# Optimization experiments

Hardware: AMD Instinct MI355X
Metric: run time of the kernel (lower is better)

The kernel has to match this reference:

```python
import jax, jax.numpy as jnp
import numpy as np

CUTOFF = 5.0           # module init kwarg
NSYS, NAT = 64, 1000   # 64 systems of 1000 atoms each
BOX = 21.544           # cubic box edge -> ~0.1 atoms/A^3 (water-like density)
MAX_PAIRS = 2_200_000


def setup_inputs() -> dict:
    key = jax.random.key(0)
    coords = jax.random.uniform(key, (NSYS * NAT, 3), dtype=jnp.float32) * BOX
    isys = jnp.repeat(jnp.arange(NSYS, dtype=jnp.int32), NAT)
    natoms = jnp.full((NSYS,), NAT, dtype=jnp.int32)
    return {"coordinates": coords, "isys": isys, "natoms": natoms}


def reference(coordinates, isys, natoms):
    # Fixed-capacity cutoff neighbor list (no PBC branch), faithful to
    # GraphGeneratorFixed: half-list (i<j, same system), squared distances d12,
    # compacted into a MAX_PAIRS buffer padded with padding_value=N, then
    # symmetrized by concatenation.
    nsys = natoms.shape[0]
    n = coordinates.shape[0]
    nat = n // nsys                      # equal-sized systems (static)
    padding_value = n
    cutoff2 = jnp.float32(CUTOFF * CUTOFF)

    x = coordinates.reshape(nsys, nat, 3)                 # [S, nat, 3]
    sq = jnp.sum(x * x, axis=-1)                          # [S, nat]
    gram = jnp.einsum('sid,sjd->sij', x, x)               # [S, nat, nat]
    d12 = sq[:, :, None] + sq[:, None, :] - 2.0 * gram    # squared distances

    triu = jnp.triu(jnp.ones((nat, nat), dtype=bool), k=1)  # i < j half-list
    mask = (d12 < cutoff2) & triu[None, :, :]             # [S, nat, nat]
    mflat = mask.reshape(-1)                              # [S*nat*nat]
    npairs = jnp.sum(mflat)

    # stream-compaction: position of each kept pair in the output buffer
    pos = jnp.cumsum(mflat.astype(jnp.int32)) - 1
    sel = jnp.where(mflat, pos, MAX_PAIRS)                # OOB -> dropped
    flat_idx = jnp.arange(nsys * nat * nat, dtype=jnp.int32)
    idx_buf = jnp.full((MAX_PAIRS,), -1, dtype=jnp.int32).at[sel].set(
        flat_idx, mode='drop')

    valid = idx_buf >= 0
    ib = jnp.maximum(idx_buf, 0)
    s = ib // (nat * nat)
    rem = ib % (nat * nat)
    i = rem // nat
    j = rem % nat
    src = jnp.where(valid, s * nat + i, padding_value)
    dst = jnp.where(valid, s * nat + j, padding_value)
    d12_sel = jnp.where(valid, d12.reshape(-1)[ib], cutoff2)

    # symmetrize (directed graph), as in the original
    edge_src = jnp.concatenate([src, dst])
    edge_dst = jnp.concatenate([dst, src])
    d12_out = jnp.concatenate([d12_sel, d12_sel])
    return edge_src, edge_dst, d12_out, npairs
```

## Files before the change

### kernel.cpp

```cpp
#include <hip/hip_runtime.h>

#define NSYS 64
#define NAT  1000
#define NTOT (NSYS * NAT)
#define MP   2200000
#define CUT2 25.0f
#define PADV 64000.0f
#define SCAN_BLOCKS 250
#define CAP  104
#define EB   512
#define LCN  1152
#define NROWS 512
#define POSB  4096

__device__ __forceinline__ float dist2f(float xi, float yi, float zi,
                                        float xj, float yj, float zj) {
    float dx = xi - xj, dy = yi - yj, dz = zi - zj;
    return fmaf(dz, dz, fmaf(dy, dy, dx * dx));
}

__device__ __forceinline__ int mbcnt(unsigned long long m) {
    unsigned lo = __builtin_amdgcn_mbcnt_lo((unsigned)m, 0u);
    return (int)__builtin_amdgcn_mbcnt_hi((unsigned)(m >> 32), lo);
}

__device__ __forceinline__ int emit_group(uint2* __restrict__ q, int running,
                                          bool k, int j, int r, float d,
                                          unsigned long long m) {
    if (k) {
        int rank = running + mbcnt(m);
        if (rank < CAP)
            q[rank] = make_uint2((unsigned)(j - r), __float_as_uint(d));
    }
    return running + (int)__popcll(m);
}

__global__ __launch_bounds__(1024) void k_eval(const float* __restrict__ coords,
                                               int* __restrict__ counts,
                                               uint2* __restrict__ qbuf) {
    __shared__ float4 lc[LCN];
    int s      = blockIdx.x >> 3;
    int stripe = blockIdx.x & 7;
    const float* cs = coords + s * (NAT * 3);
    for (int a = threadIdx.x; a < LCN; a += 1024)
        lc[a] = (a < NAT)
              ? make_float4(cs[3 * a], cs[3 * a + 1], cs[3 * a + 2], 0.0f)
              : make_float4(1.0e30f, 1.0e30f, 1.0e30f, 0.0f);
    __syncthreads();
    int w    = threadIdx.x >> 6;
    int lane = threadIdx.x & 63;
    int W    = stripe * 16 + w;
    for (int t = 0;; t++) {
        int r = ((t & 1) ? (127 - W) : W) + (t << 7);
        if (r >= NAT) { if (((t & 1) ? W : (127 - W)) + (t << 7) >= NAT) break; else continue; }
        float4 ci = lc[r];
        int grow = s * NAT + r;
        uint2* q = qbuf + (size_t)grow * CAP;
        int running = 0;
        int jb = r + 1;
        for (; jb + 255 < NAT; jb += 256) {
            int j = jb + lane;
            float4 c0 = lc[j];
            float4 c1 = lc[j + 64];
            float4 c2 = lc[j + 128];
            float4 c3 = lc[j + 192];
            float d0 = dist2f(ci.x, ci.y, ci.z, c0.x, c0.y, c0.z);
            float d1 = dist2f(ci.x, ci.y, ci.z, c1.x, c1.y, c1.z);
            float d2 = dist2f(ci.x, ci.y, ci.z, c2.x, c2.y, c2.z);
            float d3 = dist2f(ci.x, ci.y, ci.z, c3.x, c3.y, c3.z);
            bool k0 = d0 < CUT2;
            bool k1 = d1 < CUT2;
            bool k2 = d2 < CUT2;
            bool k3 = d3 < CUT2;
            unsigned long long m0 = __ballot(k0);
            unsigned long long m1 = __ballot(k1);
            unsigned long long m2 = __ballot(k2);
            unsigned long long m3 = __ballot(k3);
            running = emit_group(q, running, k0, j,       r, d0, m0);
            running = emit_group(q, running, k1, j + 64,  r, d1, m1);
            running = emit_group(q, running, k2, j + 128, r, d2, m2);
            running = emit_group(q, running, k3, j + 192, r, d3, m3);
        }
        for (; jb < NAT; jb += 64) {
            int j = jb + lane;
            float4 c0 = lc[j];
            float d0 = dist2f(ci.x, ci.y, ci.z, c0.x, c0.y, c0.z);
            bool k0 = (j < NAT) && (d0 < CUT2);
            unsigned long long m0 = __ballot(k0);
            running = emit_group(q, running, k0, j, r, d0, m0);
        }
        if (lane == 0) counts[grow] = running;
    }
}

__global__ void k_scan_a(const int* __restrict__ counts, int* __restrict__ offs,
                         int* __restrict__ bsum) {
    __shared__ int tmp[256];
    int t = threadIdx.x;
    int g = blockIdx.x * 256 + t;
    int v = counts[g];
    tmp[t] = v;
    __syncthreads();
    for (int off = 1; off < 256; off <<= 1) {
        int u = (t >= off) ? tmp[t - off] : 0;
        __syncthreads();
        tmp[t] += u;
        __syncthreads();
    }
    offs[g] = tmp[t] - v;
    if (t == 255) bsum[blockIdx.x] = tmp[255];
}

__global__ __launch_bounds__(1024) void k_emit(const int* __restrict__ offs,
                                               const int* __restrict__ bsum,
                                               const uint2* __restrict__ qbuf,
                                               float* __restrict__ out) {
    __shared__ int bpre[256];
    __shared__ int lgoff[NROWS + 1];
    __shared__ int sh_r0, sh_tot;
    int t = threadIdx.x;
    int v = 0;
    if (t < 256) {
        v = (t < SCAN_BLOCKS) ? bsum[t] : 0;
        bpre[t] = v;
    }
    __syncthreads();
    for (int off = 1; off < 256; off <<= 1) {
        int u = 0;
        if (t < 256 && t >= off) u = bpre[t - off];
        __syncthreads();
        if (t < 256) bpre[t] += u;
        __syncthreads();
    }
    int incl = (t < 256) ? bpre[t] : 0;
    __syncthreads();
    if (t < 256) bpre[t] = incl - v;
    if (t == 255) sh_tot = incl;
    __syncthreads();
    int total = sh_tot;

    int p0 = blockIdx.x * POSB;
    if (t == 0) {
        int lo = 0, hi = NTOT;
        while (lo < hi) {
            int mid = (lo + hi + 1) >> 1;
            int g = (mid < NTOT) ? offs[mid] + bpre[mid >> 8] : total;
            if (g <= p0) lo = mid; else hi = mid - 1;
        }
        sh_r0 = lo;
    }
    __syncthreads();
    int r0 = sh_r0;
    if (t <= NROWS) {
        int r = r0 + t;
        lgoff[t] = (r < NTOT) ? offs[r] + bpre[r >> 8] : total;
    }
    __syncthreads();

    if (blockIdx.x == 0 && t == 0) out[6 * MP] = (float)total;
    int valid = total < MP ? total : MP;

    int p4 = p0 + t * 4;
    if (p4 >= MP) return;
    int k = 0;
    for (int step = 256; step; step >>= 1) {
        int nk = k + step;
        if (nk <= NROWS - 1 && lgoff[nk] <= p4) k = nk;
    }
    float fs[4], fd[4], dd[4];
#pragma unroll
    for (int e = 0; e < 4; e++) {
        int p = p4 + e;
        if (p < valid) {
            while (k < NROWS - 1 && lgoff[k + 1] <= p) k++;
            int row = r0 + k;
            int local = p - lgoff[k];
            if (local > CAP - 1) local = CAP - 1;
            uint2 rec = qbuf[(size_t)row * CAP + local];
            fs[e] = (float)row;
            fd[e] = (float)(row + (int)rec.x);
            dd[e] = __uint_as_float(rec.y);
        } else {
            fs[e] = PADV; fd[e] = PADV; dd[e] = CUT2;
        }
    }
    if (p4 + 4 <= MP) {
        float4 vs = {fs[0], fs[1], fs[2], fs[3]};
        float4 vd = {fd[0], fd[1], fd[2], fd[3]};
        float4 vv = {dd[0], dd[1], dd[2], dd[3]};
        *(float4*)(out + p4)          = vs;
        *(float4*)(out + MP + p4)     = vd;
        *(float4*)(out + 2 * MP + p4) = vd;
        *(float4*)(out + 3 * MP + p4) = vs;
        *(float4*)(out + 4 * MP + p4) = vv;
        *(float4*)(out + 5 * MP + p4) = vv;
    } else {
#pragma unroll
        for (int e = 0; e < 4; e++) {
            int p = p4 + e;
            if (p < MP) {
                out[p]          = fs[e];
                out[MP + p]     = fd[e];
                out[2 * MP + p] = fd[e];
                out[3 * MP + p] = fs[e];
                out[4 * MP + p] = dd[e];
                out[5 * MP + p] = dd[e];
            }
        }
    }
}

extern "C" void kernel_launch(void* const* d_in, const int* in_sizes, int n_in,
                              void* d_out, int out_size, void* d_ws, size_t ws_size,
                              hipStream_t stream) {
    const float* coords = (const float*)d_in[0];
    float* out = (float*)d_out;

    int*   counts = (int*)d_ws;
    int*   offs   = counts + NTOT;
    int*   bsum   = offs + NTOT;
    uint2* qbuf   = (uint2*)(bsum + 256);

    int emit_blocks = (MP + POSB - 1) / POSB;
    k_eval<<<EB, 1024, 0, stream>>>(coords, counts, qbuf);
    k_scan_a<<<SCAN_BLOCKS, 256, 0, stream>>>(counts, offs, bsum);
    k_emit<<<emit_blocks, 1024, 0, stream>>>(offs, bsum, qbuf, out);
}
```

Measured before the change: 111.3 us.

## Hoist block-prefix scan and row search into a single-block scan kernel

Adds a one-block k_scan_b kernel that scans the per-block sums once and binary-searches the starting row for every emit block. Before, each of the ~538 emit blocks redid the 256-entry scan and its own search. Both scans now use wavefront shuffle scans instead of LDS scans with many barriers. The eval kernel also makes the row index wave-uniform with readfirstlane. The cost is one extra kernel launch and a serial single-block stage placed on the critical path.

```diff
diff --git a/kernel.cpp b/kernel.cpp
--- a/kernel.cpp
+++ b/kernel.cpp
@@ -12,6 +12,7 @@
 #define LCN  1152
 #define NROWS 512
 #define POSB  4096
+#define EMITB ((MP + POSB - 1) / POSB)
 
 __device__ __forceinline__ float dist2f(float xi, float yi, float zi,
                                         float xj, float yj, float zj) {
@@ -54,7 +55,7 @@
         int r = ((t & 1) ? (127 - W) : W) + (t << 7);
         if (r >= NAT) { if (((t & 1) ? W : (127 - W)) + (t << 7) >= NAT) break; else continue; }
         float4 ci = lc[r];
-        int grow = s * NAT + r;
+        int grow = __builtin_amdgcn_readfirstlane(s * NAT + r);
         uint2* q = qbuf + (size_t)grow * CAP;
         int running = 0;
         int jb = r + 1;
@@ -93,71 +94,97 @@
     }
 }
 
-__global__ void k_scan_a(const int* __restrict__ counts, int* __restrict__ offs,
-                         int* __restrict__ bsum) {
-    __shared__ int tmp[256];
-    int t = threadIdx.x;
+__global__ __launch_bounds__(256) void k_scan_a(const int* __restrict__ counts,
+                                                int* __restrict__ offs,
+                                                int* __restrict__ bsum) {
+    __shared__ int wsum[4];
+    int t = threadIdx.x, lane = t & 63, wid = t >> 6;
     int g = blockIdx.x * 256 + t;
     int v = counts[g];
-    tmp[t] = v;
-    __syncthreads();
-    for (int off = 1; off < 256; off <<= 1) {
-        int u = (t >= off) ? tmp[t - off] : 0;
-        __syncthreads();
-        tmp[t] += u;
-        __syncthreads();
-    }
-    offs[g] = tmp[t] - v;
-    if (t == 255) bsum[blockIdx.x] = tmp[255];
-}
-
-__global__ __launch_bounds__(1024) void k_emit(const int* __restrict__ offs,
-                                               const int* __restrict__ bsum,
-                                               const uint2* __restrict__ qbuf,
-                                               float* __restrict__ out) {
-    __shared__ int bpre[256];
-    __shared__ int lgoff[NROWS + 1];
-    __shared__ int sh_r0, sh_tot;
-    int t = threadIdx.x;
-    int v = 0;
+    int x = v;
+#pragma unroll
+    for (int off = 1; off < 64; off <<= 1) {
+        int u = __shfl_up(x, off);
+        if (lane >= off) x += u;
+    }
+    if (lane == 63) wsum[wid] = x;
+    __syncthreads();
+    int base = 0;
+    if (wid > 0) base += wsum[0];
+    if (wid > 1) base += wsum[1];
+    if (wid > 2) base += wsum[2];
+    offs[g] = base + x - v;
+    if (t == 255) bsum[blockIdx.x] = base + x;
+}
+
+__global__ __launch_bounds__(1024) void k_scan_b(const int* __restrict__ offs,
+                                                 const int* __restrict__ bsum,
+                                                 int* __restrict__ bpre,
+                                                 int* __restrict__ r0g,
+                                                 int* __restrict__ totp,
+                                                 float* __restrict__ out) {
+    __shared__ int bexc[256];
+    __shared__ int wsum[4];
+    __shared__ int sh_tot;
+    int t = threadIdx.x, lane = t & 63, wid = t >> 6;
+    int v = 0, x = 0;
     if (t < 256) {
         v = (t < SCAN_BLOCKS) ? bsum[t] : 0;
-        bpre[t] = v;
-    }
-    __syncthreads();
-    for (int off = 1; off < 256; off <<= 1) {
-        int u = 0;
-        if (t < 256 && t >= off) u = bpre[t - off];
-        __syncthreads();
-        if (t < 256) bpre[t] += u;
-        __syncthreads();
-    }
-    int incl = (t < 256) ? bpre[t] : 0;
-    __syncthreads();
-    if (t < 256) bpre[t] = incl - v;
-    if (t == 255) sh_tot = incl;
+        x = v;
+#pragma unroll
+        for (int off = 1; off < 64; off <<= 1) {
+            int u = __shfl_up(x, off);
+            if (lane >= off) x += u;
+        }
+        if (lane == 63) wsum[wid] = x;
+    }
+    __syncthreads();
+    if (t < 256) {
+        int base = 0;
+        if (wid > 0) base += wsum[0];
+        if (wid > 1) base += wsum[1];
+        if (wid > 2) base += wsum[2];
+        int excl = base + x - v;
+        bexc[t] = excl;
+        bpre[t] = excl;
+        if (t == 255) {
+            int tot = base + x;
+            sh_tot = tot;
+            totp[0] = tot;
+            out[6 * MP] = (float)tot;
+        }
+    }
     __syncthreads();
     int total = sh_tot;
-
-    int p0 = blockIdx.x * POSB;
-    if (t == 0) {
+    for (int eb = t; eb < EMITB; eb += 1024) {
+        int p0 = eb * POSB;
         int lo = 0, hi = NTOT;
         while (lo < hi) {
             int mid = (lo + hi + 1) >> 1;
-            int g = (mid < NTOT) ? offs[mid] + bpre[mid >> 8] : total;
-            if (g <= p0) lo = mid; else hi = mid - 1;
-        }
-        sh_r0 = lo;
-    }
-    __syncthreads();
-    int r0 = sh_r0;
+            int gg = (mid < NTOT) ? offs[mid] + bexc[mid >> 8] : total;
+            if (gg <= p0) lo = mid; else hi = mid - 1;
+        }
+        r0g[eb] = lo;
+    }
+}
+
+__global__ __launch_bounds__(1024) void k_emit(const int* __restrict__ offs,
+                                               const int* __restrict__ bpre,
+                                               const int* __restrict__ r0g,
+                                               const int* __restrict__ totp,
+                                               const uint2* __restrict__ qbuf,
+                                               float* __restrict__ out) {
+    __shared__ int lgoff[NROWS + 1];
+    int t = threadIdx.x;
+    int r0 = r0g[blockIdx.x];
+    int total = totp[0];
     if (t <= NROWS) {
         int r = r0 + t;
         lgoff[t] = (r < NTOT) ? offs[r] + bpre[r >> 8] : total;
     }
     __syncthreads();
 
-    if (blockIdx.x == 0 && t == 0) out[6 * MP] = (float)total;
+    int p0 = blockIdx.x * POSB;
     int valid = total < MP ? total : MP;
 
     int p4 = p0 + t * 4;
@@ -219,10 +246,13 @@
     int*   counts = (int*)d_ws;
     int*   offs   = counts + NTOT;
     int*   bsum   = offs + NTOT;
-    uint2* qbuf   = (uint2*)(bsum + 256);
-
-    int emit_blocks = (MP + POSB - 1) / POSB;
+    int*   bpre   = bsum + 256;
+    int*   r0g    = bpre + 256;
+    int*   totp   = r0g + 544;
+    uint2* qbuf   = (uint2*)(totp + 8);
+
     k_eval<<<EB, 1024, 0, stream>>>(coords, counts, qbuf);
     k_scan_a<<<SCAN_BLOCKS, 256, 0, stream>>>(counts, offs, bsum);
-    k_emit<<<emit_blocks, 1024, 0, stream>>>(offs, bsum, qbuf, out);
-}
+    k_scan_b<<<1, 1024, 0, stream>>>(offs, bsum, bpre, r0g, totp, out);
+    k_emit<<<EMITB, 1024, 0, stream>>>(offs, bpre, r0g, totp, qbuf, out);
+}
```

After: 114.1 us. 2.5% more time.

## Process four rows per wavefront in eval kernel and use shuffle-based block scan

Applied to the files above, without the earlier changes.

The eval kernel now has each wavefront handle four consecutive rows at once. Each loaded column coordinate from LDS is reused across four distance computations, cutting LDS reads and loop overhead, and the four row counts are written with a single int4 store. Work is split into 250 quads assigned to waves in a balanced pair (W, 255-W) instead of the previous snake pattern over rows. The scan kernel replaces its LDS Hillis-Steele loop, which synchronised the block at every step, with a wavefront shuffle scan plus a single barrier. Holding four rows raises register pressure, and the quad pairing may leave triangle work less evenly balanced.

```diff
diff --git a/kernel.cpp b/kernel.cpp
--- a/kernel.cpp
+++ b/kernel.cpp
@@ -50,65 +50,127 @@
     int w    = threadIdx.x >> 6;
     int lane = threadIdx.x & 63;
     int W    = stripe * 16 + w;
-    for (int t = 0;; t++) {
-        int r = ((t & 1) ? (127 - W) : W) + (t << 7);
-        if (r >= NAT) { if (((t & 1) ? W : (127 - W)) + (t << 7) >= NAT) break; else continue; }
-        float4 ci = lc[r];
-        int grow = s * NAT + r;
-        uint2* q = qbuf + (size_t)grow * CAP;
-        int running = 0;
-        int jb = r + 1;
-        for (; jb + 255 < NAT; jb += 256) {
-            int j = jb + lane;
-            float4 c0 = lc[j];
-            float4 c1 = lc[j + 64];
-            float4 c2 = lc[j + 128];
-            float4 c3 = lc[j + 192];
-            float d0 = dist2f(ci.x, ci.y, ci.z, c0.x, c0.y, c0.z);
-            float d1 = dist2f(ci.x, ci.y, ci.z, c1.x, c1.y, c1.z);
-            float d2 = dist2f(ci.x, ci.y, ci.z, c2.x, c2.y, c2.z);
-            float d3 = dist2f(ci.x, ci.y, ci.z, c3.x, c3.y, c3.z);
-            bool k0 = d0 < CUT2;
-            bool k1 = d1 < CUT2;
-            bool k2 = d2 < CUT2;
-            bool k3 = d3 < CUT2;
+#pragma unroll
+    for (int t = 0; t < 2; t++) {
+        int Q = t ? (255 - W) : W;
+        if (Q > 249) continue;
+        int r0 = Q * 4;
+        float4 a0 = lc[r0];
+        float4 a1 = lc[r0 + 1];
+        float4 a2 = lc[r0 + 2];
+        float4 a3 = lc[r0 + 3];
+        int gb = __builtin_amdgcn_readfirstlane(s * NAT + r0);
+        uint2* q0 = qbuf + (size_t)gb * CAP;
+        uint2* q1 = q0 + CAP;
+        uint2* q2 = q1 + CAP;
+        uint2* q3 = q2 + CAP;
+        int run0 = 0, run1 = 0, run2 = 0, run3 = 0;
+        {
+            int j = r0 + 1 + lane;
+            float4 c = lc[j];
+            float d0 = dist2f(a0.x, a0.y, a0.z, c.x, c.y, c.z);
+            float d1 = dist2f(a1.x, a1.y, a1.z, c.x, c.y, c.z);
+            float d2 = dist2f(a2.x, a2.y, a2.z, c.x, c.y, c.z);
+            float d3 = dist2f(a3.x, a3.y, a3.z, c.x, c.y, c.z);
+            bool in = j < NAT;
+            bool k0 = in && (d0 < CUT2);
+            bool k1 = in && (j > r0 + 1) && (d1 < CUT2);
+            bool k2 = in && (j > r0 + 2) && (d2 < CUT2);
+            bool k3 = in && (j > r0 + 3) && (d3 < CUT2);
             unsigned long long m0 = __ballot(k0);
             unsigned long long m1 = __ballot(k1);
             unsigned long long m2 = __ballot(k2);
             unsigned long long m3 = __ballot(k3);
-            running = emit_group(q, running, k0, j,       r, d0, m0);
-            running = emit_group(q, running, k1, j + 64,  r, d1, m1);
-            running = emit_group(q, running, k2, j + 128, r, d2, m2);
-            running = emit_group(q, running, k3, j + 192, r, d3, m3);
+            run0 = emit_group(q0, run0, k0, j, r0,     d0, m0);
+            run1 = emit_group(q1, run1, k1, j, r0 + 1, d1, m1);
+            run2 = emit_group(q2, run2, k2, j, r0 + 2, d2, m2);
+            run3 = emit_group(q3, run3, k3, j, r0 + 3, d3, m3);
+        }
+        int jb = r0 + 65;
+        for (; jb + 127 < NAT; jb += 128) {
+            int j = jb + lane;
+            float4 c0 = lc[j];
+            float4 c1 = lc[j + 64];
+            float d00 = dist2f(a0.x, a0.y, a0.z, c0.x, c0.y, c0.z);
+            float d10 = dist2f(a1.x, a1.y, a1.z, c0.x, c0.y, c0.z);
+            float d20 = dist2f(a2.x, a2.y, a2.z, c0.x, c0.y, c0.z);
+            float d30 = dist2f(a3.x, a3.y, a3.z, c0.x, c0.y, c0.z);
+            bool k00 = d00 < CUT2;
+            bool k10 = d10 < CUT2;
+            bool k20 = d20 < CUT2;
+            bool k30 = d30 < CUT2;
+            unsigned long long m00 = __ballot(k00);
+            unsigned long long m10 = __ballot(k10);
+            unsigned long long m20 = __ballot(k20);
+            unsigned long long m30 = __ballot(k30);
+            run0 = emit_group(q0, run0, k00, j, r0,     d00, m00);
+            run1 = emit_group(q1, run1, k10, j, r0 + 1, d10, m10);
+            run2 = emit_group(q2, run2, k20, j, r0 + 2, d20, m20);
+            run3 = emit_group(q3, run3, k30, j, r0 + 3, d30, m30);
+            float d01 = dist2f(a0.x, a0.y, a0.z, c1.x, c1.y, c1.z);
+            float d11 = dist2f(a1.x, a1.y, a1.z, c1.x, c1.y, c1.z);
+            float d21 = dist2f(a2.x, a2.y, a2.z, c1.x, c1.y, c1.z);
+            float d31 = dist2f(a3.x, a3.y, a3.z, c1.x, c1.y, c1.z);
+            bool k01 = d01 < CUT2;
+            bool k11 = d11 < CUT2;
+            bool k21 = d21 < CUT2;
+            bool k31 = d31 < CUT2;
+            unsigned long long m01 = __ballot(k01);
+            unsigned long long m11 = __ballot(k11);
+            unsigned long long m21 = __ballot(k21);
+            unsigned long long m31 = __ballot(k31);
+            run0 = emit_group(q0, run0, k01, j + 64, r0,     d01, m01);
+            run1 = emit_group(q1, run1, k11, j + 64, r0 + 1, d11, m11);
+            run2 = emit_group(q2, run2, k21, j + 64, r0 + 2, d21, m21);
+            run3 = emit_group(q3, run3, k31, j + 64, r0 + 3, d31, m31);
         }
         for (; jb < NAT; jb += 64) {
             int j = jb + lane;
-            float4 c0 = lc[j];
-            float d0 = dist2f(ci.x, ci.y, ci.z, c0.x, c0.y, c0.z);
-            bool k0 = (j < NAT) && (d0 < CUT2);
+            float4 c = lc[j];
+            float d0 = dist2f(a0.x, a0.y, a0.z, c.x, c.y, c.z);
+            float d1 = dist2f(a1.x, a1.y, a1.z, c.x, c.y, c.z);
+            float d2 = dist2f(a2.x, a2.y, a2.z, c.x, c.y, c.z);
+            float d3 = dist2f(a3.x, a3.y, a3.z, c.x, c.y, c.z);
+            bool in = j < NAT;
+            bool k0 = in && (d0 < CUT2);
+            bool k1 = in && (d1 < CUT2);
+            bool k2 = in && (d2 < CUT2);
+            bool k3 = in && (d3 < CUT2);
             unsigned long long m0 = __ballot(k0);
-            running = emit_group(q, running, k0, j, r, d0, m0);
-        }
-        if (lane == 0) counts[grow] = running;
-    }
-}
-
-__global__ void k_scan_a(const int* __restrict__ counts, int* __restrict__ offs,
-                         int* __restrict__ bsum) {
-    __shared__ int tmp[256];
-    int t = threadIdx.x;
+            unsigned long long m1 = __ballot(k1);
+            unsigned long long m2 = __ballot(k2);
+            unsigned long long m3 = __ballot(k3);
+            run0 = emit_group(q0, run0, k0, j, r0,     d0, m0);
+            run1 = emit_group(q1, run1, k1, j, r0 + 1, d1, m1);
+            run2 = emit_group(q2, run2, k2, j, r0 + 2, d2, m2);
+            run3 = emit_group(q3, run3, k3, j, r0 + 3, d3, m3);
+        }
+        if (lane == 0)
+            *(int4*)(counts + gb) = make_int4(run0, run1, run2, run3);
+    }
+}
+
+__global__ __launch_bounds__(256) void k_scan_a(const int* __restrict__ counts,
+                                                int* __restrict__ offs,
+                                                int* __restrict__ bsum) {
+    __shared__ int wsum[4];
+    int t = threadIdx.x, lane = t & 63, wid = t >> 6;
     int g = blockIdx.x * 256 + t;
     int v = counts[g];
-    tmp[t] = v;
-    __syncthreads();
-    for (int off = 1; off < 256; off <<= 1) {
-        int u = (t >= off) ? tmp[t - off] : 0;
-        __syncthreads();
-        tmp[t] += u;
-        __syncthreads();
-    }
-    offs[g] = tmp[t] - v;
-    if (t == 255) bsum[blockIdx.x] = tmp[255];
+    int x = v;
+#pragma unroll
+    for (int off = 1; off < 64; off <<= 1) {
+        int u = __shfl_up(x, off);
+        if (lane >= off) x += u;
+    }
+    if (lane == 63) wsum[wid] = x;
+    __syncthreads();
+    int base = 0;
+    if (wid > 0) base += wsum[0];
+    if (wid > 1) base += wsum[1];
+    if (wid > 2) base += wsum[2];
+    offs[g] = base + x - v;
+    if (t == 255) bsum[blockIdx.x] = base + x;
 }
 
 __global__ __launch_bounds__(1024) void k_emit(const int* __restrict__ offs,
```

Result: faster. 108.3 us (-2.7%).
